# Performance work log

Measured on AMD Instinct MI355X. Metric: run time of the kernel, lower is better.

The kernel has to match this reference:

```python
import jax, jax.numpy as jnp
import numpy as np

B, T, C = 2, 4096, 2048
H, K = 32, 64
C_ATT = H * K  # == C here
LAYER, N_LAYERS = 12, 24
HEAD_SIZE_DIVISOR = 8.0
EPS = 1e-5


def setup_inputs() -> dict:
    key = jax.random.key(0)
    kx, ks, kw, k1, k2, k3, k4, k5 = jax.random.split(key, 8)
    r01 = LAYER / (N_LAYERS - 1)          # ratio_0_to_1
    r10 = 1.0 - LAYER / N_LAYERS          # ratio_1_to_almost0
    ddd = np.arange(C, dtype=np.float32) / C
    n = np.arange(C_ATT, dtype=np.float32)
    decay_speed = -6.0 + 5.0 * (n / (C_ATT - 1)) ** (0.7 + 1.3 * r01)
    faaaa = (r01 * (1.0 - n / (C_ATT - 1)) + ((np.arange(C_ATT) + 1) % 3 - 1) * 0.1).astype(np.float32)
    std = 0.02
    return {
        "x": jax.random.normal(kx, (B, T, C), jnp.float32),
        "shift_state_in": jax.random.normal(ks, (B, C), jnp.float32),
        "wkv_state_in": jax.random.normal(kw, (B, H, K, K), jnp.float32) * 0.1,
        "time_mix_k": jnp.asarray(ddd ** r10),
        "time_mix_v": jnp.asarray(ddd ** r10 + 0.3 * r01),
        "time_mix_r": jnp.asarray(ddd ** (0.5 * r10)),
        "time_mix_g": jnp.asarray(ddd ** (0.5 * r10)),
        "time_decay": jnp.asarray(decay_speed.astype(np.float32).reshape(H, K)),
        "time_faaaa": jnp.asarray(faaaa.reshape(H, K)),
        "W_r": jax.random.normal(k1, (C_ATT, C), jnp.float32) * std,
        "W_k": jax.random.normal(k2, (C_ATT, C), jnp.float32) * std,
        "W_v": jax.random.normal(k3, (C_ATT, C), jnp.float32) * std,
        "W_g": jax.random.normal(k4, (C_ATT, C), jnp.float32) * std,
        "W_o": jax.random.normal(k5, (C, C_ATT), jnp.float32) * std,
        "ln_gamma": jnp.ones((C_ATT,), jnp.float32),
        "ln_beta": jnp.zeros((C_ATT,), jnp.float32),
    }


def reference(x, shift_state_in, wkv_state_in, time_mix_k, time_mix_v, time_mix_r,
              time_mix_g, time_decay, time_faaaa, W_r, W_k, W_v, W_g, W_o,
              ln_gamma, ln_beta):
    shift_state_out = x[:, -1]
    # token shift: previous-token embedding, seeded from shift_state_in
    xx = jnp.concatenate([shift_state_in[:, None, :], x[:, :-1]], axis=1)
    lerp = lambda m: x * m + xx * (1.0 - m)  # modified_lerp(x, mix, xx)
    r = (lerp(time_mix_r) @ W_r.T).reshape(B, T, H, K)
    k = (lerp(time_mix_k) @ W_k.T).reshape(B, T, H, K)
    v = (lerp(time_mix_v) @ W_v.T).reshape(B, T, H, K)
    g = jax.nn.silu(lerp(time_mix_g) @ W_g.T)  # [B,T,C_ATT]
    w = jnp.exp(-jnp.exp(time_decay.astype(jnp.float32)))  # [H,K] per-channel decay
    u = time_faaaa  # [H,K] bonus for current token

    def step(S, rkv):
        r_t, k_t, v_t = rkv  # each [B,H,K]
        a = k_t[..., :, None] * v_t[..., None, :]                       # [B,H,K,K] outer kv
        y = jnp.einsum('bhk,bhkv->bhv', r_t, S + u[None, :, :, None] * a)
        S_new = w[None, :, :, None] * S + a
        return S_new, y

    xs = (jnp.moveaxis(r, 1, 0), jnp.moveaxis(k, 1, 0), jnp.moveaxis(v, 1, 0))  # [T,B,H,K]
    wkv_state_out, y = jax.lax.scan(step, wkv_state_in, xs)  # y: [T,B,H,K]
    y = jnp.moveaxis(y, 0, 1).reshape(B, T, C_ATT)
    # GroupNorm(n_head groups) over flattened tokens, after /head_size_divisor
    yg = (y / HEAD_SIZE_DIVISOR).reshape(B * T, H, K)
    mu = yg.mean(-1, keepdims=True)
    var = yg.var(-1, keepdims=True)
    yn = ((yg - mu) * jax.lax.rsqrt(var + EPS)).reshape(B, T, C_ATT) * ln_gamma + ln_beta
    out = (yn * g) @ W_o.T
    return out, shift_state_out, wkv_state_out
```

## Files before the change

kernel.cpp:

```cpp
#include <hip/hip_runtime.h>
#include <cstdint>
#include <cstddef>

typedef unsigned short u16;
typedef __attribute__((ext_vector_type(8))) short short8;
typedef __attribute__((ext_vector_type(8))) __bf16 bf16x8;
typedef __attribute__((ext_vector_type(4))) float f32x4;

#define NB 2
#define NT 4096
#define NC 2048
#define NH 32
#define NK 64
#define NM (NB*NT)
#define LCH 64
#define NCH (NT/LCH)
#define LOG2E 1.44269504f
#define SLAB  ((size_t)NM*NC)
#define WSLAB ((size_t)NC*NC)

__device__ __forceinline__ u16 f2bf(float f) {
  union { float f; unsigned u; } x; x.f = f;
  unsigned r = x.u + 0x7FFFu + ((x.u >> 16) & 1u);
  return (u16)(r >> 16);
}
__device__ __forceinline__ float bf2f(u16 u) {
  union { unsigned u; float f; } x; x.u = ((unsigned)u) << 16; return x.f;
}
__device__ __forceinline__ void glds16(const u16* g, u16* l) {
  __builtin_amdgcn_global_load_lds(
      (const __attribute__((address_space(1))) unsigned int*)g,
      (__attribute__((address_space(3))) unsigned int*)l, 16, 0, 0);
}
#define FENCE() asm volatile("" ::: "memory")
#define BAR() do { FENCE(); __builtin_amdgcn_s_barrier(); FENCE(); } while(0)
#define MF(a, b, c) __builtin_amdgcn_mfma_f32_16x16x32_bf16((a), (b), (c), 0, 0, 0)

__global__ __launch_bounds__(256)
void cvt_w4(const float* __restrict__ Wr, const float* __restrict__ Wk,
            const float* __restrict__ Wv, const float* __restrict__ Wg,
            u16* __restrict__ dst)
{
  const int z = blockIdx.y;
  const float* src = (z==0)?Wr:(z==1)?Wk:(z==2)?Wv:Wg;
  u16* d = dst + (size_t)z * WSLAB;
  const int n8 = (int)(WSLAB / 8);
  for (int i = blockIdx.x*256 + threadIdx.x; i < n8; i += gridDim.x*256) {
    const float4 a = ((const float4*)src)[2*i];
    const float4 b = ((const float4*)src)[2*i + 1];
    short8 o;
    o[0]=(short)f2bf(a.x); o[1]=(short)f2bf(a.y); o[2]=(short)f2bf(a.z); o[3]=(short)f2bf(a.w);
    o[4]=(short)f2bf(b.x); o[5]=(short)f2bf(b.y); o[6]=(short)f2bf(b.z); o[7]=(short)f2bf(b.w);
    ((short8*)d)[i] = o;
  }
}

__global__ __launch_bounds__(256)
void cvt_w1(const float* __restrict__ W, u16* __restrict__ dst)
{
  const int n8 = (int)(WSLAB / 8);
  for (int i = blockIdx.x*256 + threadIdx.x; i < n8; i += gridDim.x*256) {
    const float4 a = ((const float4*)W)[2*i];
    const float4 b = ((const float4*)W)[2*i + 1];
    short8 o;
    o[0]=(short)f2bf(a.x); o[1]=(short)f2bf(a.y); o[2]=(short)f2bf(a.z); o[3]=(short)f2bf(a.w);
    o[4]=(short)f2bf(b.x); o[5]=(short)f2bf(b.y); o[6]=(short)f2bf(b.z); o[7]=(short)f2bf(b.w);
    ((short8*)dst)[i] = o;
  }
}

__global__ __launch_bounds__(256)
void prep_lerp1(const float* __restrict__ x, const float* __restrict__ shift,
                const float* __restrict__ mix, u16* __restrict__ dst)
{
  const int n8 = (int)(SLAB / 8);
  for (int i = blockIdx.x*256 + threadIdx.x; i < n8; i += gridDim.x*256) {
    const int m = i >> 8;
    const int c = (i & 255) * 8;
    const float* xp = x + (size_t)m*NC + c;
    const float* xxp = ((m & (NT-1)) == 0) ? (shift + (size_t)(m >> 12)*NC + c)
                                           : (xp - NC);
    float xv[8], xxv[8], mm[8];
    *(float4*)&xv[0]  = ((const float4*)xp)[0];  *(float4*)&xv[4]  = ((const float4*)xp)[1];
    *(float4*)&xxv[0] = ((const float4*)xxp)[0]; *(float4*)&xxv[4] = ((const float4*)xxp)[1];
    *(float4*)&mm[0]  = *(const float4*)&mix[c]; *(float4*)&mm[4]  = *(const float4*)&mix[c+4];
    short8 o;
#pragma unroll
    for (int j = 0; j < 8; j++) {
      const float d = xv[j] - xxv[j];
      o[j] = (short)f2bf(fmaf(mm[j], d, xxv[j]));
    }
    ((short8*)dst)[i] = o;
  }
}

__global__ __launch_bounds__(256)
void prep_lerp3(const float* __restrict__ x, const float* __restrict__ shift,
                const float* __restrict__ mixr, const float* __restrict__ mixk,
                const float* __restrict__ mixv,
                u16* __restrict__ dr, u16* __restrict__ dk, u16* __restrict__ dv)
{
  const int n8 = (int)(SLAB / 8);
  for (int i = blockIdx.x*256 + threadIdx.x; i < n8; i += gridDim.x*256) {
    const int m = i >> 8;
    const int c = (i & 255) * 8;
    const float* xp = x + (size_t)m*NC + c;
    const float* xxp = ((m & (NT-1)) == 0) ? (shift + (size_t)(m >> 12)*NC + c)
                                           : (xp - NC);
    float xv[8], xxv[8], mr[8], mk[8], mv[8];
    *(float4*)&xv[0]  = ((const float4*)xp)[0];  *(float4*)&xv[4]  = ((const float4*)xp)[1];
    *(float4*)&xxv[0] = ((const float4*)xxp)[0]; *(float4*)&xxv[4] = ((const float4*)xxp)[1];
    *(float4*)&mr[0]  = *(const float4*)&mixr[c]; *(float4*)&mr[4] = *(const float4*)&mixr[c+4];
    *(float4*)&mk[0]  = *(const float4*)&mixk[c]; *(float4*)&mk[4] = *(const float4*)&mixk[c+4];
    *(float4*)&mv[0]  = *(const float4*)&mixv[c]; *(float4*)&mv[4] = *(const float4*)&mixv[c+4];
    short8 orr, okk, ovv;
#pragma unroll
    for (int j = 0; j < 8; j++) {
      const float d = xv[j] - xxv[j];
      orr[j] = (short)f2bf(fmaf(mr[j], d, xxv[j]));
      okk[j] = (short)f2bf(fmaf(mk[j], d, xxv[j]));
      ovv[j] = (short)f2bf(fmaf(mv[j], d, xxv[j]));
    }
    ((short8*)dr)[i] = orr;
    ((short8*)dk)[i] = okk;
    ((short8*)dv)[i] = ovv;
  }
}

template<bool F32OUT>
__global__ __launch_bounds__(512, 2)
void gemm256(const u16* __restrict__ A0, const u16* __restrict__ A1,
             const u16* __restrict__ A2,
             const u16* __restrict__ B0, const u16* __restrict__ B1,
             const u16* __restrict__ B2,
             u16* __restrict__ O0, u16* __restrict__ O1, u16* __restrict__ O2,
             float* __restrict__ outf, int silu_z)
{
  const int z = blockIdx.z;
  const u16* A = (z==0)?A0:(z==1)?A1:A2;
  const u16* B = (z==0)?B0:(z==1)?B1:B2;
  u16* O       = (z==0)?O0:(z==1)?O1:O2;

  const int flat = blockIdx.y * 8 + blockIdx.x;
  const int swz  = (flat & 7) * 32 + (flat >> 3);
  const int m0 = (swz >> 3) * 256, n0 = (swz & 7) * 256;

  __shared__ __align__(16) u16 As[2*16384];
  __shared__ __align__(16) u16 Bs[2*16384];

  const int tid = threadIdx.x, w = tid >> 6, lane = tid & 63;
  const int wr = (w >> 2) * 128, wc = (w & 3) * 64;
  const int lr = lane & 15, hi = lane >> 4, hi4 = hi * 4;

  const int l8 = lane >> 3;
  const int e7 = lane & 7;
  const u16* agp = A + (size_t)(m0 + w*32 + l8) * NC + (size_t)((e7 ^ l8) * 8);
  const u16* bgp = B + (size_t)(n0 + w*32 + l8) * NC + (size_t)((e7 ^ l8) * 8);
  const int ldst = w * 2048;

  const int es = lr & 7;
  const int cs0 = ((hi    ) ^ es) * 8;
  const int cs1 = ((hi + 4) ^ es) * 8;
  const int rbA = (wr + lr) * 64;
  const int rbB = (wc + lr) * 64;

  f32x4 acc[8][4] = {};

#define STAGE(buf, s) do {                                            \
    const u16* a_ = agp + (size_t)(s) * 64;                           \
    const u16* b_ = bgp + (size_t)(s) * 64;                           \
    _Pragma("unroll")                                                 \
    for (int i = 0; i < 4; i++) {                                     \
      glds16(a_ + (size_t)i*8*NC, &As[(buf)*16384 + ldst + i*512]);   \
      glds16(b_ + (size_t)i*8*NC, &Bs[(buf)*16384 + ldst + i*512]);   \
    } } while(0)

#define LDA(buf, mi, kk) __builtin_bit_cast(bf16x8, *(const short8*)  \
    &As[(buf)*16384 + rbA + (mi)*1024 + ((kk) ? cs1 : cs0)])
#define LDB(buf, nj, kk) __builtin_bit_cast(bf16x8, *(const short8*)  \
    &Bs[(buf)*16384 + rbB + (nj)*1024 + ((kk) ? cs1 : cs0)])

#define HALF(buf, mb) do {                                            \
    bf16x8 af[4][2];                                                  \
    _Pragma("unroll")                                                 \
    for (int mi = 0; mi < 4; mi++) {                                  \
      af[mi][0] = LDA(buf, (mb)+mi, 0);                               \
      af[mi][1] = LDA(buf, (mb)+mi, 1); }                             \
    __builtin_amdgcn_s_setprio(1);                                    \
    _Pragma("unroll")                                                 \
    for (int mi = 0; mi < 4; mi++)                                    \
      _Pragma("unroll")                                               \
      for (int nj = 0; nj < 4; nj++) {                                \
        acc[(mb)+mi][nj] = MF(af[mi][0], bfr[nj][0], acc[(mb)+mi][nj]); \
        acc[(mb)+mi][nj] = MF(af[mi][1], bfr[nj][1], acc[(mb)+mi][nj]); } \
    __builtin_amdgcn_s_setprio(0); } while(0)

#define KTILE(buf, kt, DOSTAGE, VM) do {                              \
    asm volatile("s_waitcnt vmcnt(" #VM ")" ::: "memory");            \
    BAR();                                                            \
    bf16x8 bfr[4][2];                                                 \
    _Pragma("unroll")                                                 \
    for (int nj = 0; nj < 4; nj++) {                                  \
      bfr[nj][0] = LDB(buf, nj, 0);                                   \
      bfr[nj][1] = LDB(buf, nj, 1); }                                 \
    HALF(buf, 0);                                                     \
    HALF(buf, 4);                                                     \
    BAR();                                                            \
    if (DOSTAGE) STAGE(buf, (kt) + 2);                                \
  } while(0)

  STAGE(0, 0);
  STAGE(1, 1);

#pragma unroll 1
  for (int kt = 0; kt < 30; kt += 2) {
    KTILE(0, kt,   true, 8);
    KTILE(1, kt+1, true, 8);
  }
  KTILE(0, 30, false, 8);
  KTILE(1, 31, false, 0);
#undef KTILE
#undef HALF
#undef LDA
#undef LDB
#undef STAGE

  const bool do_silu = (z == silu_z);
#pragma unroll
  for (int mi = 0; mi < 8; mi++) {
    const int grow0 = m0 + wr + mi*16 + hi4;
#pragma unroll
    for (int nj = 0; nj < 4; nj++) {
      const int gcol = n0 + wc + nj*16 + lr;
#pragma unroll
      for (int j = 0; j < 4; j++) {
        float v = acc[mi][nj][j];
        if constexpr (F32OUT) {
          outf[(size_t)(grow0 + j) * NC + gcol] = v;
        } else {
          if (do_silu) v = v / (1.f + expf(-v));
          O[(size_t)(grow0 + j) * NC + gcol] = f2bf(v);
        }
      }
    }
  }
}

__global__ __launch_bounds__(256, 2)
void gemm_rkvg(const float* __restrict__ x, const float* __restrict__ shiftst,
               const float* __restrict__ mixr, const float* __restrict__ mixk,
               const float* __restrict__ mixv, const float* __restrict__ mixg,
               const float* __restrict__ Wr, const float* __restrict__ Wk,
               const float* __restrict__ Wv, const float* __restrict__ Wg,
               u16* __restrict__ outr, u16* __restrict__ outk,
               u16* __restrict__ outv, u16* __restrict__ outg)
{
  const int z = blockIdx.z;
  const float* mix = (z==0) ? mixr : (z==1) ? mixk : (z==2) ? mixv : mixg;
  const float* W   = (z==0) ? Wr   : (z==1) ? Wk   : (z==2) ? Wv   : Wg;
  u16* out         = (z==0) ? outr : (z==1) ? outk : (z==2) ? outv : outg;

  __shared__ __align__(16) u16 As[128][40];
  __shared__ __align__(16) u16 Bs[128][40];

  const int tid  = threadIdx.x;
  const int m0   = blockIdx.y * 128;
  const int n0   = blockIdx.x * 128;
  const int srow = tid >> 3;
  const int c4   = (tid & 7) * 4;
  const int lane = tid & 63;
  const int wid  = tid >> 6;
  const int wr   = (wid >> 1) * 64;
  const int wc   = (wid & 1) * 64;
  const int lr   = lane & 15;
  const int ko   = (lane >> 4) * 8;

  f32x4 acc[4][4] = {};

  for (int c0 = 0; c0 < NC; c0 += 32) {
    float4 xa[4], xxa[4], wa[4];
    const float4 mv4 = *(const float4*)&mix[c0 + c4];
#pragma unroll
    for (int i = 0; i < 4; i++) {
      const int row = srow + i*32;
      const int m = m0 + row;
      const float* xp = x + (size_t)m * NC + c0 + c4;
      xa[i] = *(const float4*)xp;
      const float* xxp = ((m & (NT-1)) == 0)
                       ? (shiftst + (size_t)(m >> 12) * NC + c0 + c4)
                       : (xp - NC);
      xxa[i] = *(const float4*)xxp;
      wa[i]  = *(const float4*)(W + (size_t)(n0 + row) * NC + c0 + c4);
    }
    __syncthreads();
#pragma unroll
    for (int i = 0; i < 4; i++) {
      const int row = srow + i*32;
      const float a0 = xxa[i].x + mv4.x * (xa[i].x - xxa[i].x);
      const float a1 = xxa[i].y + mv4.y * (xa[i].y - xxa[i].y);
      const float a2 = xxa[i].z + mv4.z * (xa[i].z - xxa[i].z);
      const float a3 = xxa[i].w + mv4.w * (xa[i].w - xxa[i].w);
      uint2 pa, pb;
      pa.x = (unsigned)f2bf(a0) | ((unsigned)f2bf(a1) << 16);
      pa.y = (unsigned)f2bf(a2) | ((unsigned)f2bf(a3) << 16);
      pb.x = (unsigned)f2bf(wa[i].x) | ((unsigned)f2bf(wa[i].y) << 16);
      pb.y = (unsigned)f2bf(wa[i].z) | ((unsigned)f2bf(wa[i].w) << 16);
      *(uint2*)&As[row][c4] = pa;
      *(uint2*)&Bs[row][c4] = pb;
    }
    __syncthreads();
    bf16x8 af[4], bfr[4];
#pragma unroll
    for (int mi = 0; mi < 4; mi++)
      af[mi] = __builtin_bit_cast(bf16x8, *(const short8*)&As[wr + mi*16 + lr][ko]);
#pragma unroll
    for (int nj = 0; nj < 4; nj++)
      bfr[nj] = __builtin_bit_cast(bf16x8, *(const short8*)&Bs[wc + nj*16 + lr][ko]);
#pragma unroll
    for (int mi = 0; mi < 4; mi++)
#pragma unroll
      for (int nj = 0; nj < 4; nj++)
        acc[mi][nj] = MF(af[mi], bfr[nj], acc[mi][nj]);
  }

  const bool do_silu = (z == 3);
#pragma unroll
  for (int mi = 0; mi < 4; mi++) {
    const int grow0 = m0 + wr + mi*16 + (lane >> 4) * 4;
#pragma unroll
    for (int nj = 0; nj < 4; nj++) {
      const int gcol = n0 + wc + nj*16 + lr;
#pragma unroll
      for (int j = 0; j < 4; j++) {
        float v = acc[mi][nj][j];
        if (do_silu) v = v / (1.f + expf(-v));
        out[(size_t)(grow0 + j) * NC + gcol] = f2bf(v);
      }
    }
  }
}

__global__ __launch_bounds__(256, 2)
void gemm_out_k(const u16* __restrict__ A, const float* __restrict__ Wo,
                float* __restrict__ out)
{
  __shared__ __align__(16) u16 As[128][40];
  __shared__ __align__(16) u16 Bs[128][40];
  const int tid  = threadIdx.x;
  const int m0 = blockIdx.y * 128, n0 = blockIdx.x * 128;
  const int arow = tid >> 2;
  const int ac8  = (tid & 3) * 8;
  const int srow = tid >> 3;
  const int c4   = (tid & 7) * 4;
  const int lane = tid & 63, wid = tid >> 6;
  const int wr = (wid >> 1) * 64, wc = (wid & 1) * 64;
  const int lr = lane & 15, ko = (lane >> 4) * 8;

  f32x4 acc[4][4] = {};

  for (int c0 = 0; c0 < NC; c0 += 32) {
    uint4 av[2]; float4 wv[4];
#pragma unroll
    for (int i = 0; i < 2; i++)
      av[i] = *(const uint4*)(A + (size_t)(m0 + arow + i*64) * NC + c0 + ac8);
#pragma unroll
    for (int i = 0; i < 4; i++)
      wv[i] = *(const float4*)(Wo + (size_t)(n0 + srow + i*32) * NC + c0 + c4);
    __syncthreads();
#pragma unroll
    for (int i = 0; i < 2; i++)
      *(uint4*)&As[arow + i*64][ac8] = av[i];
#pragma unroll
    for (int i = 0; i < 4; i++) {
      uint2 pb;
      pb.x = (unsigned)f2bf(wv[i].x) | ((unsigned)f2bf(wv[i].y) << 16);
      pb.y = (unsigned)f2bf(wv[i].z) | ((unsigned)f2bf(wv[i].w) << 16);
      *(uint2*)&Bs[srow + i*32][c4] = pb;
    }
    __syncthreads();
    bf16x8 af[4], bfr[4];
#pragma unroll
    for (int mi = 0; mi < 4; mi++)
      af[mi] = __builtin_bit_cast(bf16x8, *(const short8*)&As[wr + mi*16 + lr][ko]);
#pragma unroll
    for (int nj = 0; nj < 4; nj++)
      bfr[nj] = __builtin_bit_cast(bf16x8, *(const short8*)&Bs[wc + nj*16 + lr][ko]);
#pragma unroll
    for (int mi = 0; mi < 4; mi++)
#pragma unroll
      for (int nj = 0; nj < 4; nj++)
        acc[mi][nj] = MF(af[mi], bfr[nj], acc[mi][nj]);
  }

#pragma unroll
  for (int mi = 0; mi < 4; mi++) {
    const int grow0 = m0 + wr + mi*16 + (lane >> 4) * 4;
#pragma unroll
    for (int nj = 0; nj < 4; nj++) {
      const int gcol = n0 + wc + nj*16 + lr;
#pragma unroll
      for (int j = 0; j < 4; j++)
        out[(size_t)(grow0 + j) * NC + gcol] = acc[mi][nj][j];
    }
  }
}

__global__ __launch_bounds__(256, 2)
void wkv_intra(const u16* __restrict__ rbuf, u16* __restrict__ kbuf, u16* __restrict__ vbuf,
               const float* __restrict__ decay, const float* __restrict__ faaaa)
{
  const int blk = blockIdx.x;
  const int c  = blk & (NCH-1);
  const int bh = blk >> 6;
  const int b = bh >> 5, h = bh & 31;

  __shared__ __align__(16) u16 RBs[64][72];
  __shared__ __align__(16) u16 KBs[64][72];
  __shared__ __align__(16) u16 K2t[64][72];
  __shared__ __align__(16) u16 Vt[64][72];
  __shared__ __align__(16) u16 Asm[64][72];
  __shared__ float ds[64];

  const int tid = threadIdx.x;
  const int row = tid >> 2;
  const int c16 = (tid & 3) * 16;

  const size_t gbase = ((size_t)b*NT + (size_t)c*LCH) * NC + h*NK;

  float l2w[16], uu[16];
#pragma unroll
  for (int j = 0; j < 16; j++) {
    l2w[j] = -__expf(decay[h*NK + c16 + j]) * LOG2E;
    uu[j]  = faaaa[h*NK + c16 + j];
  }

  const u16* rp = rbuf + gbase + (size_t)row*NC + c16;
  const u16* kp = kbuf + gbase + (size_t)row*NC + c16;
  const u16* vp = vbuf + gbase + (size_t)row*NC + c16;
  short8 r8[2], k8[2], v8[2];
  r8[0] = *(const short8*)rp;       r8[1] = *(const short8*)(rp+8);
  k8[0] = *(const short8*)kp;       k8[1] = *(const short8*)(kp+8);
  v8[0] = *(const short8*)vp;       v8[1] = *(const short8*)(vp+8);

  float dp = 0.f;
  short8 rb8[2], kb8[2];
#pragma unroll
  for (int half = 0; half < 2; half++) {
#pragma unroll
    for (int j = 0; j < 8; j++) {
      const int e = half*8 + j;
      const float rf = bf2f((u16)r8[half][j]);
      const float kf = bf2f((u16)k8[half][j]);
      dp += rf * uu[e] * kf;
      rb8[half][j] = (short)f2bf(rf * exp2f(l2w[e] * (float)row));
      kb8[half][j] = (short)f2bf(kf * exp2f(-l2w[e] * (float)(row + 1)));
      K2t[c16 + e][row] = f2bf(kf * exp2f(l2w[e] * (float)(63 - row)));
      Vt[c16 + e][row]  = (u16)v8[half][j];
    }
    *(short8*)&RBs[row][c16 + half*8] = rb8[half];
    *(short8*)&KBs[row][c16 + half*8] = kb8[half];
  }
  dp += __shfl_xor(dp, 1);
  dp += __shfl_xor(dp, 2);
  if ((tid & 3) == 0) ds[row] = dp;
  __syncthreads();

  const int lane = tid & 63, w = tid >> 6;
  const int lr = lane & 15, ko = (lane >> 4) * 8, hi = lane >> 4;

  f32x4 accA[4] = {};
  {
    const bf16x8 a0 = __builtin_bit_cast(bf16x8, *(const short8*)&RBs[16*w + lr][ko]);
    const bf16x8 a1 = __builtin_bit_cast(bf16x8, *(const short8*)&RBs[16*w + lr][32 + ko]);
#pragma unroll
    for (int jt = 0; jt < 4; jt++) {
      const bf16x8 b0 = __builtin_bit_cast(bf16x8, *(const short8*)&KBs[16*jt + lr][ko]);
      const bf16x8 b1 = __builtin_bit_cast(bf16x8, *(const short8*)&KBs[16*jt + lr][32 + ko]);
      accA[jt] = MF(a0, b0, accA[jt]);
      accA[jt] = MF(a1, b1, accA[jt]);
    }
  }
#pragma unroll
  for (int jt = 0; jt < 4; jt++) {
#pragma unroll
    for (int reg = 0; reg < 4; reg++) {
      const int i = 16*w + hi*4 + reg;
      const int j = 16*jt + lr;
      const float val = (j < i) ? accA[jt][reg] : ((j == i) ? ds[i] : 0.f);
      Asm[i][j] = f2bf(val);
    }
  }
  __syncthreads();

  f32x4 accP[4] = {}, accG[4] = {};
  {
    const bf16x8 ap0 = __builtin_bit_cast(bf16x8, *(const short8*)&Asm[16*w + lr][ko]);
    const bf16x8 ap1 = __builtin_bit_cast(bf16x8, *(const short8*)&Asm[16*w + lr][32 + ko]);
    const bf16x8 ag0 = __builtin_bit_cast(bf16x8, *(const short8*)&K2t[16*w + lr][ko]);
    const bf16x8 ag1 = __builtin_bit_cast(bf16x8, *(const short8*)&K2t[16*w + lr][32 + ko]);
#pragma unroll
    for (int vt = 0; vt < 4; vt++) {
      const bf16x8 bv0 = __builtin_bit_cast(bf16x8, *(const short8*)&Vt[16*vt + lr][ko]);
      const bf16x8 bv1 = __builtin_bit_cast(bf16x8, *(const short8*)&Vt[16*vt + lr][32 + ko]);
      accP[vt] = MF(ap0, bv0, accP[vt]);
      accP[vt] = MF(ap1, bv1, accP[vt]);
      accG[vt] = MF(ag0, bv0, accG[vt]);
      accG[vt] = MF(ag1, bv1, accG[vt]);
    }
  }
#pragma unroll
  for (int vt = 0; vt < 4; vt++) {
#pragma unroll
    for (int reg = 0; reg < 4; reg++) {
      const int ir = 16*w + hi*4 + reg;
      const int iv = 16*vt + lr;
      vbuf[gbase + (size_t)ir*NC + iv] = f2bf(accP[vt][reg]);
      kbuf[gbase + (size_t)ir*NC + iv] = f2bf(accG[vt][reg]);
    }
  }
}

__global__ __launch_bounds__(256)
void wkv_scan2(u16* __restrict__ kbuf, const float* __restrict__ wkv_in,
               const float* __restrict__ decay, float* __restrict__ state_out)
{
  const int bh = blockIdx.x, b = bh >> 5, h = bh & 31;
  const int tid = threadIdx.x;
  const int kq = tid >> 2, v16 = (tid & 3) * 16;
  const float l2w = -__expf(decay[h*NK + kq]) * LOG2E;
  const float w64 = exp2f(l2w * 64.f);

  float S[16];
  const size_t sbase = ((size_t)bh*NK + kq)*NK + v16;
#pragma unroll
  for (int j = 0; j < 16; j++) S[j] = wkv_in[sbase + j];

  size_t gb = (size_t)b*NT*NC + h*NK + (size_t)kq*NC + v16;
  const size_t cstride = (size_t)LCH * NC;

  short8 pa = *(const short8*)(kbuf + gb);
  short8 pb = *(const short8*)(kbuf + gb + 8);
  for (int cc = 0; cc < NCH; cc++) {
    const short8 ga = pa, gb8 = pb;
    if (cc + 1 < NCH) {
      pa = *(const short8*)(kbuf + gb + cstride);
      pb = *(const short8*)(kbuf + gb + cstride + 8);
    }
    short8 sa, sb;
#pragma unroll
    for (int j = 0; j < 8; j++) { sa[j] = (short)f2bf(S[j]); sb[j] = (short)f2bf(S[8+j]); }
    *(short8*)(kbuf + gb) = sa;
    *(short8*)(kbuf + gb + 8) = sb;
#pragma unroll
    for (int j = 0; j < 8; j++) {
      S[j]   = fmaf(w64, S[j],   bf2f((u16)ga[j]));
      S[8+j] = fmaf(w64, S[8+j], bf2f((u16)gb8[j]));
    }
    gb += cstride;
  }
#pragma unroll
  for (int j = 0; j < 16; j++) state_out[sbase + j] = S[j];
}

__global__ __launch_bounds__(256, 2)
void wkv_cross(u16* __restrict__ rybuf, const u16* __restrict__ kbuf,
               const u16* __restrict__ vbuf, const float* __restrict__ decay)
{
  const int blk = blockIdx.x;
  const int c  = blk & (NCH-1);
  const int bh = blk >> 6;
  const int b = bh >> 5, h = bh & 31;

  __shared__ __align__(16) u16 RBs[64][72];
  __shared__ __align__(16) u16 St[64][72];

  const int tid = threadIdx.x;
  const int row = tid >> 2;
  const int c16 = (tid & 3) * 16;
  const size_t gbase = ((size_t)b*NT + (size_t)c*LCH) * NC + h*NK;

  float l2w[16];
#pragma unroll
  for (int j = 0; j < 16; j++)
    l2w[j] = -__expf(decay[h*NK + c16 + j]) * LOG2E;

  const u16* sp = kbuf + gbase + (size_t)row*NC + c16;
  short8 s8a = *(const short8*)sp, s8b = *(const short8*)(sp + 8);
#pragma unroll
  for (int j = 0; j < 8; j++) {
    St[c16 + j][row]     = (u16)s8a[j];
    St[c16 + 8 + j][row] = (u16)s8b[j];
  }
  const u16* rp = rybuf + gbase + (size_t)row*NC + c16;
  short8 r8a = *(const short8*)rp, r8b = *(const short8*)(rp + 8);
  short8 ra, rb;
#pragma unroll
  for (int j = 0; j < 8; j++) {
    ra[j] = (short)f2bf(bf2f((u16)r8a[j]) * exp2f(l2w[j] * (float)row));
    rb[j] = (short)f2bf(bf2f((u16)r8b[j]) * exp2f(l2w[8+j] * (float)row));
  }
  *(short8*)&RBs[row][c16]     = ra;
  *(short8*)&RBs[row][c16 + 8] = rb;
  __syncthreads();

  const int lane = tid & 63, w = tid >> 6;
  const int lr = lane & 15, ko = (lane >> 4) * 8, hi = lane >> 4;

  f32x4 acc[4] = {};
  const bf16x8 a0 = __builtin_bit_cast(bf16x8, *(const short8*)&RBs[16*w + lr][ko]);
  const bf16x8 a1 = __builtin_bit_cast(bf16x8, *(const short8*)&RBs[16*w + lr][32 + ko]);
#pragma unroll
  for (int vt = 0; vt < 4; vt++) {
    const bf16x8 b0 = __builtin_bit_cast(bf16x8, *(const short8*)&St[16*vt + lr][ko]);
    const bf16x8 b1 = __builtin_bit_cast(bf16x8, *(const short8*)&St[16*vt + lr][32 + ko]);
    acc[vt] = MF(a0, b0, acc[vt]);
    acc[vt] = MF(a1, b1, acc[vt]);
  }
#pragma unroll
  for (int vt = 0; vt < 4; vt++) {
#pragma unroll
    for (int reg = 0; reg < 4; reg++) {
      const int ir = 16*w + hi*4 + reg;
      const int iv = 16*vt + lr;
      const size_t a = gbase + (size_t)ir*NC + iv;
      rybuf[a] = f2bf(acc[vt][reg] + bf2f(vbuf[a]));
    }
  }
}

__global__ __launch_bounds__(256)
void gnorm_k(const u16* __restrict__ ybuf, u16* __restrict__ gbuf,
             const float* __restrict__ gamma, const float* __restrict__ beta)
{
  const int wid = threadIdx.x >> 6, lane = threadIdx.x & 63;
  const int g = blockIdx.x * 4 + wid;
  const int idx = g * 64 + lane;
  const float yv = bf2f(ybuf[idx]) * 0.125f;
  float s1 = yv, s2 = yv * yv;
#pragma unroll
  for (int m = 32; m; m >>= 1) { s1 += __shfl_xor(s1, m, 64); s2 += __shfl_xor(s2, m, 64); }
  const float mu  = s1 * (1.f/64.f);
  const float var = s2 * (1.f/64.f) - mu*mu;
  const float rstd = rsqrtf(var + 1e-5f);
  const int ch = (g & (NH-1)) * NK + lane;
  const float yn = (yv - mu) * rstd * gamma[ch] + beta[ch];
  gbuf[idx] = f2bf(yn * bf2f(gbuf[idx]));
}

__global__ void shift_copy(const float* __restrict__ x, float* __restrict__ o)
{
  const int i = blockIdx.x * 256 + threadIdx.x;
  if (i < NB*NC) {
    const int b = i >> 11, c = i & (NC-1);
    o[i] = x[((size_t)b*NT + (NT-1)) * NC + c];
  }
}

extern "C" void kernel_launch(void* const* d_in, const int* in_sizes, int n_in,
                              void* d_out, int out_size, void* d_ws, size_t ws_size,
                              hipStream_t stream)
{
  const float* x      = (const float*)d_in[0];
  const float* shift  = (const float*)d_in[1];
  const float* wkv_in = (const float*)d_in[2];
  const float* mixk   = (const float*)d_in[3];
  const float* mixv   = (const float*)d_in[4];
  const float* mixr   = (const float*)d_in[5];
  const float* mixg   = (const float*)d_in[6];
  const float* decay  = (const float*)d_in[7];
  const float* faaaa  = (const float*)d_in[8];
  const float* Wr     = (const float*)d_in[9];
  const float* Wk     = (const float*)d_in[10];
  const float* Wv     = (const float*)d_in[11];
  const float* Wg     = (const float*)d_in[12];
  const float* Wo     = (const float*)d_in[13];
  const float* gamma  = (const float*)d_in[14];
  const float* beta   = (const float*)d_in[15];

  float* out       = (float*)d_out;
  float* shift_out = out + (size_t)NM * NC;
  float* state_out = shift_out + NB * NC;

  u16* rbuf = (u16*)d_ws;
  u16* kbuf = rbuf + SLAB;
  u16* vbuf = kbuf + SLAB;
  u16* gbuf = vbuf + SLAB;
  u16* wbf  = gbuf + SLAB;
  u16* a0   = wbf  + SLAB;
  u16* a1   = a0   + SLAB;

  const size_t needA = 7 * SLAB * sizeof(u16);
  const size_t needB = 6 * SLAB * sizeof(u16);

  const bool fast = (ws_size >= needB);

  if (fast) {
    cvt_w4<<<dim3(512, 4), 256, 0, stream>>>(Wr, Wk, Wv, Wg, wbf);
    const u16* vb;
    if (ws_size >= needA) {
      prep_lerp3<<<dim3(2048), 256, 0, stream>>>(x, shift, mixr, mixk, mixv,
                                                 a0, a1, vbuf);
      gemm256<false><<<dim3(8, 32, 3), 512, 0, stream>>>(
          a0, a1, a0,
          wbf, wbf + WSLAB, wbf + 3*WSLAB,
          rbuf, kbuf, gbuf, nullptr, 2);
      gemm256<false><<<dim3(8, 32, 1), 512, 0, stream>>>(
          vbuf, vbuf, vbuf, wbf + 2*WSLAB, nullptr, nullptr,
          a0, nullptr, nullptr, nullptr, -1);
      vb = a0;
    } else {
      prep_lerp1<<<dim3(2048), 256, 0, stream>>>(x, shift, mixr, a0);
      gemm256<false><<<dim3(8, 32, 2), 512, 0, stream>>>(
          a0, a0, a0, wbf, wbf + 3*WSLAB, nullptr,
          rbuf, gbuf, nullptr, nullptr, 1);
      prep_lerp1<<<dim3(2048), 256, 0, stream>>>(x, shift, mixk, a0);
      gemm256<false><<<dim3(8, 32, 1), 512, 0, stream>>>(
          a0, a0, a0, wbf + WSLAB, nullptr, nullptr,
          kbuf, nullptr, nullptr, nullptr, -1);
      prep_lerp1<<<dim3(2048), 256, 0, stream>>>(x, shift, mixv, a0);
      gemm256<false><<<dim3(8, 32, 1), 512, 0, stream>>>(
          a0, a0, a0, wbf + 2*WSLAB, nullptr, nullptr,
          vbuf, nullptr, nullptr, nullptr, -1);
      vb = vbuf;
    }
    u16* vbm = (u16*)vb;
    wkv_intra<<<dim3(NB*NH*NCH), 256, 0, stream>>>(rbuf, kbuf, vbm, decay, faaaa);
    wkv_scan2<<<dim3(NB*NH), 256, 0, stream>>>(kbuf, wkv_in, decay, state_out);
    wkv_cross<<<dim3(NB*NH*NCH), 256, 0, stream>>>(rbuf, kbuf, vbm, decay);
    cvt_w1<<<dim3(512), 256, 0, stream>>>(Wo, kbuf);
    shift_copy<<<dim3((NB*NC + 255) / 256), 256, 0, stream>>>(x, shift_out);
    gnorm_k<<<dim3(NB*NT*NH/4), 256, 0, stream>>>(rbuf, gbuf, gamma, beta);
    gemm256<true><<<dim3(8, 32, 1), 512, 0, stream>>>(
        gbuf, gbuf, gbuf, kbuf, nullptr, nullptr,
        nullptr, nullptr, nullptr, out, -1);
  } else {
    gemm_rkvg<<<dim3(16, 64, 4), 256, 0, stream>>>(x, shift, mixr, mixk, mixv, mixg,
                                                   Wr, Wk, Wv, Wg, rbuf, kbuf, vbuf, gbuf);
    wkv_intra<<<dim3(NB*NH*NCH), 256, 0, stream>>>(rbuf, kbuf, vbuf, decay, faaaa);
    wkv_scan2<<<dim3(NB*NH), 256, 0, stream>>>(kbuf, wkv_in, decay, state_out);
    wkv_cross<<<dim3(NB*NH*NCH), 256, 0, stream>>>(rbuf, kbuf, vbuf, decay);
    shift_copy<<<dim3((NB*NC + 255) / 256), 256, 0, stream>>>(x, shift_out);
    gnorm_k<<<dim3(NB*NT*NH/4), 256, 0, stream>>>(rbuf, gbuf, gamma, beta);
    gemm_out_k<<<dim3(16, 64), 256, 0, stream>>>(gbuf, Wo, out);
  }
}
```

Before: 553.7 us.

## Restructure GEMM k-tile into four barrier-synced phases with split A/B staging

```diff
diff --git a/kernel.cpp b/kernel.cpp
--- a/kernel.cpp
+++ b/kernel.cpp
@@ -151,12 +151,12 @@
   const int tid = threadIdx.x, w = tid >> 6, lane = tid & 63;
   const int wr = (w >> 2) * 128, wc = (w & 3) * 64;
   const int lr = lane & 15, hi = lane >> 4, hi4 = hi * 4;
-
-  const int l8 = lane >> 3;
-  const int e7 = lane & 7;
-  const u16* agp = A + (size_t)(m0 + w*32 + l8) * NC + (size_t)((e7 ^ l8) * 8);
-  const u16* bgp = B + (size_t)(n0 + w*32 + l8) * NC + (size_t)((e7 ^ l8) * 8);
-  const int ldst = w * 2048;
+  const int l8 = lane >> 3, e7 = lane & 7;
+
+  const int arow0 = (w >> 2) * 128 + (w & 3) * 16;
+  const u16* agA = A + (size_t)(m0 + arow0 + l8) * NC + (size_t)((e7 ^ l8) * 8);
+  const int brow0 = w * 32;
+  const u16* bgB = B + (size_t)(n0 + brow0 + l8) * NC + (size_t)((e7 ^ l8) * 8);
 
   const int es = lr & 7;
   const int cs0 = ((hi    ) ^ es) * 8;
@@ -166,64 +166,98 @@
 
   f32x4 acc[8][4] = {};
 
-#define STAGE(buf, s) do {                                            \
-    const u16* a_ = agp + (size_t)(s) * 64;                           \
-    const u16* b_ = bgp + (size_t)(s) * 64;                           \
-    _Pragma("unroll")                                                 \
-    for (int i = 0; i < 4; i++) {                                     \
-      glds16(a_ + (size_t)i*8*NC, &As[(buf)*16384 + ldst + i*512]);   \
-      glds16(b_ + (size_t)i*8*NC, &Bs[(buf)*16384 + ldst + i*512]);   \
-    } } while(0)
-
-#define LDA(buf, mi, kk) __builtin_bit_cast(bf16x8, *(const short8*)  \
+#define STAGE_A(buf, s, p) do {                                         \
+    _Pragma("unroll")                                                   \
+    for (int i_ = 0; i_ < 2; i_++)                                      \
+      glds16(agA + (size_t)((p)*64 + i_*8) * NC + (size_t)(s) * 64,     \
+             &As[(buf)*16384 + (arow0 + (p)*64 + i_*8) * 64]);          \
+  } while(0)
+
+#define STAGE_B(buf, s) do {                                            \
+    _Pragma("unroll")                                                   \
+    for (int i_ = 0; i_ < 4; i_++)                                      \
+      glds16(bgB + (size_t)(i_*8) * NC + (size_t)(s) * 64,              \
+             &Bs[(buf)*16384 + (brow0 + i_*8) * 64]);                   \
+  } while(0)
+
+#define LDA(buf, mi, kk) __builtin_bit_cast(bf16x8, *(const short8*)    \
     &As[(buf)*16384 + rbA + (mi)*1024 + ((kk) ? cs1 : cs0)])
-#define LDB(buf, nj, kk) __builtin_bit_cast(bf16x8, *(const short8*)  \
+#define LDB(buf, nj, kk) __builtin_bit_cast(bf16x8, *(const short8*)    \
     &Bs[(buf)*16384 + rbB + (nj)*1024 + ((kk) ? cs1 : cs0)])
 
-#define HALF(buf, mb) do {                                            \
-    bf16x8 af[4][2];                                                  \
-    _Pragma("unroll")                                                 \
-    for (int mi = 0; mi < 4; mi++) {                                  \
-      af[mi][0] = LDA(buf, (mb)+mi, 0);                               \
-      af[mi][1] = LDA(buf, (mb)+mi, 1); }                             \
-    __builtin_amdgcn_s_setprio(1);                                    \
-    _Pragma("unroll")                                                 \
-    for (int mi = 0; mi < 4; mi++)                                    \
-      _Pragma("unroll")                                               \
-      for (int nj = 0; nj < 4; nj++) {                                \
-        acc[(mb)+mi][nj] = MF(af[mi][0], bfr[nj][0], acc[(mb)+mi][nj]); \
-        acc[(mb)+mi][nj] = MF(af[mi][1], bfr[nj][1], acc[(mb)+mi][nj]); } \
-    __builtin_amdgcn_s_setprio(0); } while(0)
-
-#define KTILE(buf, kt, DOSTAGE, VM) do {                              \
-    asm volatile("s_waitcnt vmcnt(" #VM ")" ::: "memory");            \
-    BAR();                                                            \
-    bf16x8 bfr[4][2];                                                 \
-    _Pragma("unroll")                                                 \
-    for (int nj = 0; nj < 4; nj++) {                                  \
-      bfr[nj][0] = LDB(buf, nj, 0);                                   \
-      bfr[nj][1] = LDB(buf, nj, 1); }                                 \
-    HALF(buf, 0);                                                     \
-    HALF(buf, 4);                                                     \
-    BAR();                                                            \
-    if (DOSTAGE) STAGE(buf, (kt) + 2);                                \
+#define LGKM0() do {                                                    \
+    asm volatile("s_waitcnt lgkmcnt(0)" ::: "memory");                  \
+    __builtin_amdgcn_sched_barrier(0);                                  \
   } while(0)
 
-  STAGE(0, 0);
-  STAGE(1, 1);
+#define MM(mb, AF, BF) do {                                             \
+    __builtin_amdgcn_s_setprio(1);                                      \
+    _Pragma("unroll")                                                   \
+    for (int mi_ = 0; mi_ < 4; mi_++)                                   \
+      _Pragma("unroll")                                                 \
+      for (int nj_ = 0; nj_ < 4; nj_++)                                 \
+        acc[(mb)+mi_][nj_] = MF(AF[mi_], BF[nj_], acc[(mb)+mi_][nj_]);  \
+    __builtin_amdgcn_s_setprio(0);                                      \
+  } while(0)
+
+#define KTILE(buf, kt, S01, S23, VMEND) do {                            \
+    bf16x8 bfr0[4], bfr1[4], af[4];                                     \
+                                                                \
+    _Pragma("unroll")                                                   \
+    for (int j_ = 0; j_ < 4; j_++) { bfr0[j_] = LDB(buf, j_, 0);        \
+                                     af[j_]   = LDA(buf, j_, 0); }      \
+    if (S01) STAGE_A((buf)^1, (kt)+1, 1);                               \
+    BAR(); LGKM0();                                                     \
+    MM(0, af, bfr0);                                                    \
+    BAR();                                                              \
+                                                                \
+    _Pragma("unroll")                                                   \
+    for (int j_ = 0; j_ < 4; j_++) { bfr1[j_] = LDB(buf, j_, 1);        \
+                                     af[j_]   = LDA(buf, j_, 1); }      \
+    BAR(); LGKM0();                                                     \
+    MM(0, af, bfr1);                                                    \
+    BAR();                                                              \
+                                                                \
+    _Pragma("unroll")                                                   \
+    for (int j_ = 0; j_ < 4; j_++) af[j_] = LDA(buf, 4 + j_, 0);        \
+    if (S23) STAGE_A(buf, (kt)+2, 0);                                   \
+    BAR(); LGKM0();                                                     \
+    MM(4, af, bfr0);                                                    \
+    BAR();                                                              \
+                                                                \
+    _Pragma("unroll")                                                   \
+    for (int j_ = 0; j_ < 4; j_++) af[j_] = LDA(buf, 4 + j_, 1);        \
+    if (S23) STAGE_B(buf, (kt)+2);                                      \
+    BAR(); LGKM0();                                                     \
+    MM(4, af, bfr1);                                                    \
+    VMEND;                                                              \
+    BAR();                                                              \
+  } while(0)
+
+#define VM6 asm volatile("s_waitcnt vmcnt(6)" ::: "memory")
+#define VM0 asm volatile("s_waitcnt vmcnt(0)" ::: "memory")
+
+  STAGE_A(0, 0, 0); STAGE_A(0, 0, 1); STAGE_B(0, 0);
+  STAGE_A(1, 1, 0); STAGE_B(1, 1);
+  VM6;
+  BAR();
 
 #pragma unroll 1
   for (int kt = 0; kt < 30; kt += 2) {
-    KTILE(0, kt,   true, 8);
-    KTILE(1, kt+1, true, 8);
-  }
-  KTILE(0, 30, false, 8);
-  KTILE(1, 31, false, 0);
+    KTILE(0, kt,   1, 1, VM6);
+    KTILE(1, kt+1, 1, 1, VM6);
+  }
+  KTILE(0, 30, 1, 0, VM0);
+  KTILE(1, 31, 0, 0, );
 #undef KTILE
-#undef HALF
+#undef MM
+#undef LGKM0
 #undef LDA
 #undef LDB
-#undef STAGE
+#undef STAGE_A
+#undef STAGE_B
+#undef VM6
+#undef VM0
 
   const bool do_silu = (z == silu_z);
 #pragma unroll
```

After: 570.0 us. +3.0%, slower.
